# Optimization experiments

Hardware: AMD Instinct MI355X
Metric: run time of the kernel (lower is better)

The kernel has to match this reference:

```python
import jax, jax.numpy as jnp
import numpy as np

H = 8          # head_count
C = 512        # emb_dim
DH = C // H    # head_emb_size = 64
FF = 4 * C     # feed_forward hidden = 2048
EPS = 1e-5     # nn.LayerNorm default eps


def setup_inputs() -> dict:
    key = jax.random.key(0)
    ks = jax.random.split(key, 16)
    s = lambda fan_in: 1.0 / np.sqrt(fan_in)
    inp = {
        "x": jax.random.normal(ks[0], (4, 2048, C), dtype=jnp.float32),
        "ln1_g": jnp.ones((C,), jnp.float32),
        "ln1_b": jnp.zeros((C,), jnp.float32),
        # per-head QKV projections, stacked over heads: [H, C, DH]
        "Wq": jax.random.uniform(ks[1], (H, C, DH), jnp.float32, -s(C), s(C)),
        "bq": jax.random.uniform(ks[2], (H, DH), jnp.float32, -s(C), s(C)),
        "Wk": jax.random.uniform(ks[3], (H, C, DH), jnp.float32, -s(C), s(C)),
        "bk": jax.random.uniform(ks[4], (H, DH), jnp.float32, -s(C), s(C)),
        "Wv": jax.random.uniform(ks[5], (H, C, DH), jnp.float32, -s(C), s(C)),
        "bv": jax.random.uniform(ks[6], (H, DH), jnp.float32, -s(C), s(C)),
        "Wp": jax.random.uniform(ks[7], (C, C), jnp.float32, -s(C), s(C)),
        "bp": jax.random.uniform(ks[8], (C,), jnp.float32, -s(C), s(C)),
        "ln2_g": jnp.ones((C,), jnp.float32),
        "ln2_b": jnp.zeros((C,), jnp.float32),
        "W1": jax.random.uniform(ks[9], (C, FF), jnp.float32, -s(C), s(C)),
        "b1": jax.random.uniform(ks[10], (FF,), jnp.float32, -s(C), s(C)),
        "W2": jax.random.uniform(ks[11], (FF, C), jnp.float32, -s(FF), s(FF)),
        "b2": jax.random.uniform(ks[12], (C,), jnp.float32, -s(FF), s(FF)),
    }
    return inp


def _layernorm(x, g, b):
    mu = jnp.mean(x, axis=-1, keepdims=True)
    var = jnp.mean((x - mu) ** 2, axis=-1, keepdims=True)
    return (x - mu) * jax.lax.rsqrt(var + EPS) * g + b


def _block(x, ln1_g, ln1_b, Wq, bq, Wk, bk, Wv, bv, Wp, bp, ln2_g, ln2_b, W1, b1, W2, b2):
    B, T, _ = x.shape
    h = _layernorm(x, ln1_g, ln1_b)
    # per-head projections, vectorized over heads: [B,H,T,DH]
    Q = jnp.einsum("btc,hcd->bhtd", h, Wq) + bq[None, :, None, :]
    K = jnp.einsum("btc,hcd->bhtd", h, Wk) + bk[None, :, None, :]
    V = jnp.einsum("btc,hcd->bhtd", h, Wv) + bv[None, :, None, :]
    wei = jnp.einsum("bhtd,bhsd->bhts", Q, K) / jnp.sqrt(jnp.float32(DH))
    causal = jnp.tril(jnp.ones((T, T), dtype=bool))
    wei = jnp.where(causal, wei, jnp.float32(-1e9))  # masked_fill(-1e9)
    wei = jax.nn.softmax(wei, axis=-1)
    out = jnp.einsum("bhts,bhsd->bhtd", wei, V)      # [B,H,T,DH]
    # concat heads (head order = ModuleList order) -> [B,T,C]
    out = out.transpose(0, 2, 1, 3).reshape(B, T, H * DH)
    attn = out @ Wp + bp
    x = x + attn
    h2 = _layernorm(x, ln2_g, ln2_b)
    ff = jax.nn.relu(h2 @ W1 + b1) @ W2 + b2
    return x + ff


def reference(x, ln1_g, ln1_b, Wq, bq, Wk, bk, Wv, bv, Wp, bp, ln2_g, ln2_b, W1, b1, W2, b2):
    return _block(x, ln1_g, ln1_b, Wq, bq, Wk, bk, Wv, bv, Wp, bp, ln2_g, ln2_b, W1, b1, W2, b2)
```

## Files before the change

### kernel.cpp

```cpp
#include <hip/hip_runtime.h>

typedef unsigned short u16;
typedef unsigned int   u32;
typedef __attribute__((ext_vector_type(4))) int   i32x4;
typedef __attribute__((ext_vector_type(4))) float f32x4;
typedef __attribute__((ext_vector_type(4))) unsigned short u16x4;
typedef __attribute__((ext_vector_type(8))) unsigned short u16x8;

#define DEVI static __device__ __forceinline__

DEVI u16 f2b(float f) {
  u32 u = __builtin_bit_cast(u32, f);
  return (u16)((u + 0x7FFFu + ((u >> 16) & 1u)) >> 16);
}

DEVI void mfma16(f32x4& d, i32x4 a, i32x4 b) {
  asm("v_mfma_f32_16x16x32_bf16 %0, %1, %2, %0" : "+v"(d) : "v"(a), "v"(b));
}

DEVI void gload16(const void* g, void* l) {
  __builtin_amdgcn_global_load_lds(
      (const __attribute__((address_space(1))) void*)g,
      (__attribute__((address_space(3))) void*)l, 16, 0, 0);
}

DEVI int swz(int row, int b) {
  return (row << 7) + (((b >> 4) ^ (row & 7)) << 4) + (b & 15);
}

__global__ __launch_bounds__(256) void trans_tile(
    const float* __restrict__ src, u16* __restrict__ dst, int R, int C)
{
  __shared__ u16 tile[64][72];
  const int rb = blockIdx.x * 64, cb = blockIdx.y * 64;
  const int t = threadIdx.x;
  const int tr = t >> 2, tc = (t & 3) * 16;
  const float* sp = src + (size_t)(rb + tr) * C + cb + tc;
  #pragma unroll
  for (int q = 0; q < 4; q++) {
    float4 v = *(const float4*)(sp + q * 4);
    tile[tr][tc + q*4 + 0] = f2b(v.x);
    tile[tr][tc + q*4 + 1] = f2b(v.y);
    tile[tr][tc + q*4 + 2] = f2b(v.z);
    tile[tr][tc + q*4 + 3] = f2b(v.w);
  }
  __syncthreads();
  const int dc = t >> 2, dr = (t & 3) * 16;
  u16x8 o0, o1;
  #pragma unroll
  for (int j = 0; j < 8; j++) { o0[j] = tile[dr + j][dc]; o1[j] = tile[dr + 8 + j][dc]; }
  u16* dp = dst + (size_t)(cb + dc) * R + rb + dr;
  *(u16x8*)(dp) = o0;
  *(u16x8*)(dp + 8) = o1;
}

__global__ __launch_bounds__(256) void pack_qkv_tile(
    const float* __restrict__ Wq, const float* __restrict__ Wk,
    const float* __restrict__ Wv, u16* __restrict__ dst)
{
  __shared__ u16 tile[64][72];
  const int bid = blockIdx.x;
  const int cb = (bid & 7) * 64, h = (bid >> 3) & 7, widx = bid >> 6;
  const float* W = (widx == 0) ? Wq : (widx == 1) ? Wk : Wv;
  const float* src = W + (size_t)h * 512 * 64;
  const int t = threadIdx.x;
  const int tr = t >> 2, tc = (t & 3) * 16;
  const float* sp = src + (size_t)(cb + tr) * 64 + tc;
  #pragma unroll
  for (int q = 0; q < 4; q++) {
    float4 v = *(const float4*)(sp + q * 4);
    tile[tr][tc + q*4 + 0] = f2b(v.x);
    tile[tr][tc + q*4 + 1] = f2b(v.y);
    tile[tr][tc + q*4 + 2] = f2b(v.z);
    tile[tr][tc + q*4 + 3] = f2b(v.w);
  }
  __syncthreads();
  const int dc = t >> 2, dr = (t & 3) * 16;
  u16x8 o0, o1;
  #pragma unroll
  for (int j = 0; j < 8; j++) { o0[j] = tile[dr + j][dc]; o1[j] = tile[dr + 8 + j][dc]; }
  u16* dp = dst + (size_t)(widx * 512 + h * 64 + dc) * 512 + cb + dr;
  *(u16x8*)(dp) = o0;
  *(u16x8*)(dp + 8) = o1;
}

__global__ __launch_bounds__(256) void ln_kernel(
    const float* __restrict__ x, const float* __restrict__ gamma,
    const float* __restrict__ beta, u16* __restrict__ out)
{
  const int lane = threadIdx.x & 63;
  const int row = blockIdx.x * 4 + (threadIdx.x >> 6);
  const float4* xr = (const float4*)(x + (size_t)row * 512) + lane * 2;
  float4 a0 = xr[0], a1 = xr[1];
  float s  = a0.x + a0.y + a0.z + a0.w + a1.x + a1.y + a1.z + a1.w;
  float sq = a0.x*a0.x + a0.y*a0.y + a0.z*a0.z + a0.w*a0.w
           + a1.x*a1.x + a1.y*a1.y + a1.z*a1.z + a1.w*a1.w;
  #pragma unroll
  for (int o = 32; o > 0; o >>= 1) { s += __shfl_xor(s, o); sq += __shfl_xor(sq, o); }
  const float mu = s * (1.0f / 512.0f);
  const float rstd = rsqrtf(sq * (1.0f / 512.0f) - mu * mu + 1e-5f);
  const float4* g4 = (const float4*)gamma + lane * 2;
  const float4* b4 = (const float4*)beta  + lane * 2;
  float4 g0 = g4[0], g1 = g4[1], b0 = b4[0], b1 = b4[1];
  float xv[8] = {a0.x,a0.y,a0.z,a0.w,a1.x,a1.y,a1.z,a1.w};
  float gv[8] = {g0.x,g0.y,g0.z,g0.w,g1.x,g1.y,g1.z,g1.w};
  float bv[8] = {b0.x,b0.y,b0.z,b0.w,b1.x,b1.y,b1.z,b1.w};
  u16x8 ov;
  #pragma unroll
  for (int j = 0; j < 8; j++) ov[j] = f2b((xv[j] - mu) * rstd * gv[j] + bv[j]);
  *(u16x8*)(out + (size_t)row * 512 + lane * 8) = ov;
}

template<int KD, int EPI>
__global__ __launch_bounds__(256) void gemm_bt(
    const u16* __restrict__ A, const u16* __restrict__ Bt,
    const float* __restrict__ bias0, const float* __restrict__ bias1,
    const float* __restrict__ bias2, const float* __restrict__ resid,
    void* __restrict__ out0, void* __restrict__ out1, void* __restrict__ out2)
{
  __shared__ __align__(16) u16 sA[3][128 * 32];
  __shared__ __align__(16) u16 sB[3][128 * 32];
  constexpr int NSTEP = KD / 32;
  const int tid = threadIdx.x, lane = tid & 63, w = tid >> 6;
  const int m0 = blockIdx.x * 128, n0 = blockIdx.y * 128;
  const int wr = w >> 1, wc = w & 1, r = lane & 15, gq = lane >> 4;

  f32x4 acc[4][4] = {};

  const int o0 = w * 2048 + lane * 16;
  const int row0 = o0 >> 6, kb0 = o0 & 63;
  const int o1 = o0 + 1024;
  const int row1 = o1 >> 6, kb1 = o1 & 63;
  const char* Ab = (const char*)A;
  const char* Bb = (const char*)Bt;

#define STAGE(step, buf) do {                                                \
    const int kbyte_ = (step) * 64;                                          \
    char* sAd_ = (char*)sA + (buf) * 8192 + w * 2048;                        \
    char* sBd_ = (char*)sB + (buf) * 8192 + w * 2048;                        \
    gload16(Ab + (size_t)(m0 + row0) * (KD * 2) + kbyte_ + kb0, sAd_);       \
    gload16(Ab + (size_t)(m0 + row1) * (KD * 2) + kbyte_ + kb1, sAd_ + 1024);\
    gload16(Bb + (size_t)(n0 + row0) * (KD * 2) + kbyte_ + kb0, sBd_);       \
    gload16(Bb + (size_t)(n0 + row1) * (KD * 2) + kbyte_ + kb1, sBd_ + 1024);\
  } while (0)

  STAGE(0, 0);
  STAGE(1, 1);

  for (int t = 0; t < NSTEP; t++) {
    __builtin_amdgcn_sched_barrier(0);
    __builtin_amdgcn_s_barrier();
    if (t + 2 < NSTEP) {
      STAGE(t + 2, (t + 2) % 3);
      asm volatile("s_waitcnt vmcnt(8)" ::: "memory");
    } else if (t + 1 < NSTEP) {
      asm volatile("s_waitcnt vmcnt(4)" ::: "memory");
    } else {
      asm volatile("s_waitcnt vmcnt(0)" ::: "memory");
    }
    __builtin_amdgcn_sched_barrier(0);
    __builtin_amdgcn_s_barrier();
    const u16* sAc = sA[t % 3];
    const u16* sBc = sB[t % 3];
    i32x4 af[4], bfr[4];
    #pragma unroll
    for (int i = 0; i < 4; i++)
      af[i] = *(const i32x4*)(sAc + (wr * 64 + i * 16 + r) * 32 + gq * 8);
    #pragma unroll
    for (int j = 0; j < 4; j++)
      bfr[j] = *(const i32x4*)(sBc + (wc * 64 + j * 16 + r) * 32 + gq * 8);
    #pragma unroll
    for (int i = 0; i < 4; i++)
      #pragma unroll
      for (int j = 0; j < 4; j++)
        mfma16(acc[i][j], af[i], bfr[j]);
  }
#undef STAGE

  #pragma unroll
  for (int i = 0; i < 4; i++) {
    #pragma unroll
    for (int j = 0; j < 4; j++) {
      const int mb = m0 + wr * 64 + i * 16 + gq * 4;
      const int nc = n0 + wc * 64 + j * 16 + r;
      #pragma unroll
      for (int e = 0; e < 4; e++) {
        const int m = mb + e;
        float v = acc[i][j][e];
        if (EPI == 0) {
          float bias; u16* dst;
          if (nc < 512)       { bias = bias0[nc];        dst = (u16*)out0; }
          else if (nc < 1024) { bias = bias1[nc - 512];  dst = (u16*)out1; }
          else                { bias = bias2[nc - 1024]; dst = (u16*)out2; }
          v += bias;
          const int nn = nc & 511, h = nn >> 6, d = nn & 63;
          const int bb = m >> 11, tt = m & 2047;
          dst[(size_t)((bb * 8 + h) * 2048 + tt) * 64 + d] = f2b(v);
        } else if (EPI == 1) {
          v += bias0[nc] + resid[(size_t)m * 512 + nc];
          ((float*)out0)[(size_t)m * 512 + nc] = v;
        } else {
          v += bias0[nc];
          v = fmaxf(v, 0.0f);
          ((u16*)out0)[(size_t)m * 2048 + nc] = f2b(v);
        }
      }
    }
  }
}

__global__ __launch_bounds__(256) void attn_kernel(
    const u16* __restrict__ Q, const u16* __restrict__ K,
    const u16* __restrict__ V, u16* __restrict__ O)
{
  __shared__ __align__(16) char lds[40960];
  const int tid = threadIdx.x, lane = tid & 63, w = tid >> 6;
  const int p = blockIdx.x & 15, bh = blockIdx.x >> 4;
  const int r = lane & 15, gq = lane >> 4;
  const u16* Qb = Q + (size_t)bh * (2048 * 64);
  const u16* Kb = K + (size_t)bh * (2048 * 64);
  const u16* Vb = V + (size_t)bh * (2048 * 64);
  const int bb = bh >> 3, hh = bh & 7;
  char* Pb = lds + 32768 + w * 2048;

  const int sv = (tid & 15) * 4;
  const int dv = (tid >> 4) * 4;
  u16x4 vr[4];

#define STAGEK(s0g, buf) do {                                              \
    _Pragma("unroll")                                                      \
    for (int i_ = 0; i_ < 2; i_++) {                                       \
      int o_ = w * 2048 + i_ * 1024 + lane * 16;                           \
      int so_ = o_ ^ (((o_ >> 7) & 7) << 4);                               \
      gload16((const char*)(Kb + (size_t)(s0g) * 64) + so_,                \
              lds + (buf) * 8192 + w * 2048 + i_ * 1024);                  \
    } } while (0)

#define LOADV(s0g) do {                                                    \
    _Pragma("unroll")                                                      \
    for (int j_ = 0; j_ < 4; j_++)                                         \
      vr[j_] = *(const u16x4*)(Vb + (size_t)((s0g) + sv + j_) * 64 + dv);  \
    } while (0)

#define WRITEV(buf) do {                                                   \
    _Pragma("unroll")                                                      \
    for (int dd_ = 0; dd_ < 4; dd_++) {                                    \
      u16x4 val_ = {vr[0][dd_], vr[1][dd_], vr[2][dd_], vr[3][dd_]};       \
      *(u16x4*)(lds + 16384 + (buf) * 8192 + swz(dv + dd_, sv * 2)) = val_;\
    } } while (0)

  #pragma unroll 1
  for (int half = 0; half < 2; half++) {
    const int qt = half ? p : (31 - p);
    const int q0 = qt << 6;
    const int qg = q0 + w * 16 + r;

    i32x4 qf[2];
    qf[0] = *(const i32x4*)(Qb + (size_t)(q0 + w * 16 + r) * 64 + gq * 8);
    qf[1] = *(const i32x4*)(Qb + (size_t)(q0 + w * 16 + r) * 64 + 32 + gq * 8);

    STAGEK(0, 0);
    LOADV(0);
    WRITEV(0);
    __syncthreads();

    f32x4 accO[4] = {};
    float m_run = -1e30f, l_run = 0.0f;

    for (int t = 0; t <= qt; t++) {
      const int cb = t & 1, nb = cb ^ 1;
      const bool diag = (t == qt);
      const int s0 = t << 6;
      if (!diag) {
        STAGEK(s0 + 64, nb);
        LOADV(s0 + 64);
      }

      f32x4 st[4] = {};
      const int sbmax = diag ? (w + 1) : 4;
      #pragma unroll
      for (int kd = 0; kd < 2; kd++)
        #pragma unroll
        for (int sb = 0; sb < 4; sb++)
          if (sb < sbmax) {
            i32x4 kf = *(const i32x4*)(lds + cb * 8192 + swz(sb * 16 + r, kd * 64 + gq * 16));
            mfma16(st[sb], kf, qf[kd]);
          }

      float tmax = -1e30f;
      if (diag) {
        #pragma unroll
        for (int sb = 0; sb < 4; sb++)
          #pragma unroll
          for (int e = 0; e < 4; e++) {
            int sg = s0 + sb * 16 + gq * 4 + e;
            float v = st[sb][e] * 0.125f;
            v = (sg <= qg) ? v : -1e30f;
            st[sb][e] = v;
            tmax = fmaxf(tmax, v);
          }
      } else {
        #pragma unroll
        for (int sb = 0; sb < 4; sb++)
          #pragma unroll
          for (int e = 0; e < 4; e++) {
            float v = st[sb][e] * 0.125f;
            st[sb][e] = v;
            tmax = fmaxf(tmax, v);
          }
      }
      tmax = fmaxf(tmax, __shfl_xor(tmax, 16));
      tmax = fmaxf(tmax, __shfl_xor(tmax, 32));

      if (!__all(tmax <= m_run)) {
        const float mnew = fmaxf(m_run, tmax);
        const float alpha = __expf(m_run - mnew);
        l_run *= alpha;
        float ae[4];
        #pragma unroll
        for (int e = 0; e < 4; e++) ae[e] = __shfl(alpha, gq * 4 + e);
        #pragma unroll
        for (int db = 0; db < 4; db++)
          #pragma unroll
          for (int e = 0; e < 4; e++) accO[db][e] *= ae[e];
        m_run = mnew;
      }
      float rsum = 0.0f;
      #pragma unroll
      for (int sb = 0; sb < 4; sb++)
        #pragma unroll
        for (int e = 0; e < 4; e++) {
          float pv = __expf(st[sb][e] - m_run);
          st[sb][e] = pv;
          rsum += pv;
        }
      rsum += __shfl_xor(rsum, 16);
      rsum += __shfl_xor(rsum, 32);
      l_run += rsum;

      #pragma unroll
      for (int sb = 0; sb < 4; sb++) {
        u32 lo, hi;
        asm("v_cvt_pk_bf16_f32 %0, %1, %2" : "=v"(lo) : "v"(st[sb][0]), "v"(st[sb][1]));
        asm("v_cvt_pk_bf16_f32 %0, %1, %2" : "=v"(hi) : "v"(st[sb][2]), "v"(st[sb][3]));
        uint2 pk; pk.x = lo; pk.y = hi;
        *(uint2*)(Pb + swz(r, sb * 32 + gq * 8)) = pk;
      }

      const int kmax = diag ? ((w >> 1) + 1) : 2;
      #pragma unroll
      for (int ks = 0; ks < 2; ks++)
        if (ks < kmax) {
          i32x4 pf = *(const i32x4*)(Pb + swz(r, ks * 64 + gq * 16));
          #pragma unroll
          for (int db = 0; db < 4; db++) {
            i32x4 vf = *(const i32x4*)(lds + 16384 + cb * 8192 + swz(db * 16 + r, ks * 64 + gq * 16));
            mfma16(accO[db], pf, vf);
          }
        }

      if (!diag) WRITEV(nb);
      __syncthreads();
    }

    float le[4];
    #pragma unroll
    for (int e = 0; e < 4; e++) le[e] = 1.0f / __shfl(l_run, gq * 4 + e);
    #pragma unroll
    for (int db = 0; db < 4; db++)
      #pragma unroll
      for (int e = 0; e < 4; e++) {
        int qrow = q0 + w * 16 + gq * 4 + e;
        int d = db * 16 + r;
        O[(size_t)(bb * 2048 + qrow) * 512 + hh * 64 + d] = f2b(accO[db][e] * le[e]);
      }
  }
#undef STAGEK
#undef LOADV
#undef WRITEV
}

extern "C" void kernel_launch(void* const* d_in, const int* in_sizes, int n_in,
                              void* d_out, int out_size, void* d_ws, size_t ws_size,
                              hipStream_t stream)
{
  const float* x    = (const float*)d_in[0];
  const float* ln1g = (const float*)d_in[1];
  const float* ln1b = (const float*)d_in[2];
  const float* Wq   = (const float*)d_in[3];
  const float* bq   = (const float*)d_in[4];
  const float* Wk   = (const float*)d_in[5];
  const float* bk   = (const float*)d_in[6];
  const float* Wv   = (const float*)d_in[7];
  const float* bv   = (const float*)d_in[8];
  const float* Wp   = (const float*)d_in[9];
  const float* bp   = (const float*)d_in[10];
  const float* ln2g = (const float*)d_in[11];
  const float* ln2b = (const float*)d_in[12];
  const float* W1   = (const float*)d_in[13];
  const float* b1   = (const float*)d_in[14];
  const float* W2   = (const float*)d_in[15];
  const float* b2   = (const float*)d_in[16];

  char* ws = (char*)d_ws;
  const size_t MB = 1ull << 20;
  float* x1  = (float*)(ws);
  u16* hbuf  = (u16*)(ws + 16 * MB);
  u16* Qb    = (u16*)(ws + 24 * MB);
  u16* Kb    = (u16*)(ws + 32 * MB);
  u16* Vb    = (u16*)(ws + 40 * MB);
  u16* attn  = (u16*)(ws + 48 * MB);
  u16* fbuf  = (u16*)(ws + 24 * MB);
  u16* Wqkv  = (u16*)(ws + 56 * MB);
  u16* Wpt   = (u16*)(ws + 58 * MB);
  u16* W1t   = (u16*)(ws + 59 * MB);
  u16* W2t   = (u16*)(ws + 61 * MB);
  float* outf = (float*)d_out;

  pack_qkv_tile<<<192, 256, 0, stream>>>(Wq, Wk, Wv, Wqkv);
  trans_tile<<<dim3(8, 8),  256, 0, stream>>>(Wp, Wpt, 512, 512);
  trans_tile<<<dim3(8, 32), 256, 0, stream>>>(W1, W1t, 512, 2048);
  trans_tile<<<dim3(32, 8), 256, 0, stream>>>(W2, W2t, 2048, 512);
  ln_kernel<<<2048, 256, 0, stream>>>(x, ln1g, ln1b, hbuf);
  gemm_bt<512, 0><<<dim3(64, 12), 256, 0, stream>>>(hbuf, Wqkv, bq, bk, bv,
                                                    nullptr, Qb, Kb, Vb);
  attn_kernel<<<512, 256, 0, stream>>>(Qb, Kb, Vb, attn);
  gemm_bt<512, 1><<<dim3(64, 4), 256, 0, stream>>>(attn, Wpt, bp, nullptr, nullptr,
                                                   x, x1, nullptr, nullptr);
  ln_kernel<<<2048, 256, 0, stream>>>(x1, ln2g, ln2b, hbuf);
  gemm_bt<512, 2><<<dim3(64, 16), 256, 0, stream>>>(hbuf, W1t, b1, nullptr, nullptr,
                                                    nullptr, fbuf, nullptr, nullptr);
  gemm_bt<2048, 1><<<dim3(64, 4), 256, 0, stream>>>(fbuf, W2t, b2, nullptr, nullptr,
                                                    x1, outf, nullptr, nullptr);
}
```

Measured before the change: 177.6 us.

## Remap GEMM blocks across XCDs, raise MFMA priority, use exp2 in softmax

GEMM launches move to a 1D grid with a block-index remap, so consecutive tiles that share A rows land on the same XCD chiplet and hit its L2. The MFMA loop is wrapped in s_setprio to favour matrix issue over other waves. In attention, the softmax scale folds in log2(e) and exp is computed with the hardware v_exp_f32 (exp2) instead of __expf, saving a multiply per element. The remap assumes the grid size is a multiple of 8. The raw v_exp_f32 may handle denormals or extreme inputs slightly differently.

```diff
diff --git a/kernel.cpp b/kernel.cpp
--- a/kernel.cpp
+++ b/kernel.cpp
@@ -12,6 +12,12 @@
 DEVI u16 f2b(float f) {
   u32 u = __builtin_bit_cast(u32, f);
   return (u16)((u + 0x7FFFu + ((u >> 16) & 1u)) >> 16);
+}
+
+DEVI float exp2_hw(float x) {
+  float r;
+  asm("v_exp_f32 %0, %1" : "=v"(r) : "v"(x));
+  return r;
 }
 
 DEVI void mfma16(f32x4& d, i32x4 a, i32x4 b) {
@@ -111,7 +117,7 @@
   *(u16x8*)(out + (size_t)row * 512 + lane * 8) = ov;
 }
 
-template<int KD, int EPI>
+template<int KD, int NT, int EPI>
 __global__ __launch_bounds__(256) void gemm_bt(
     const u16* __restrict__ A, const u16* __restrict__ Bt,
     const float* __restrict__ bias0, const float* __restrict__ bias1,
@@ -121,8 +127,10 @@
   __shared__ __align__(16) u16 sA[3][128 * 32];
   __shared__ __align__(16) u16 sB[3][128 * 32];
   constexpr int NSTEP = KD / 32;
+  constexpr int CPX = (64 * NT) / 8;
   const int tid = threadIdx.x, lane = tid & 63, w = tid >> 6;
-  const int m0 = blockIdx.x * 128, n0 = blockIdx.y * 128;
+  const int wg = (blockIdx.x & 7) * CPX + (blockIdx.x >> 3);
+  const int m0 = (wg / NT) * 128, n0 = (wg % NT) * 128;
   const int wr = w >> 1, wc = w & 1, r = lane & 15, gq = lane >> 4;
 
   f32x4 acc[4][4] = {};
@@ -169,11 +177,13 @@
     #pragma unroll
     for (int j = 0; j < 4; j++)
       bfr[j] = *(const i32x4*)(sBc + (wc * 64 + j * 16 + r) * 32 + gq * 8);
+    __builtin_amdgcn_s_setprio(1);
     #pragma unroll
     for (int i = 0; i < 4; i++)
       #pragma unroll
       for (int j = 0; j < 4; j++)
         mfma16(acc[i][j], af[i], bfr[j]);
+    __builtin_amdgcn_s_setprio(0);
   }
 #undef STAGE
 
@@ -226,6 +236,7 @@
   const int sv = (tid & 15) * 4;
   const int dv = (tid >> 4) * 4;
   u16x4 vr[4];
+  const float SC2 = 0.125f * 1.44269504f;
 
 #define STAGEK(s0g, buf) do {                                              \
     _Pragma("unroll")                                                      \
@@ -294,7 +305,7 @@
           #pragma unroll
           for (int e = 0; e < 4; e++) {
             int sg = s0 + sb * 16 + gq * 4 + e;
-            float v = st[sb][e] * 0.125f;
+            float v = st[sb][e] * SC2;
             v = (sg <= qg) ? v : -1e30f;
             st[sb][e] = v;
             tmax = fmaxf(tmax, v);
@@ -304,7 +315,7 @@
         for (int sb = 0; sb < 4; sb++)
           #pragma unroll
           for (int e = 0; e < 4; e++) {
-            float v = st[sb][e] * 0.125f;
+            float v = st[sb][e] * SC2;
             st[sb][e] = v;
             tmax = fmaxf(tmax, v);
           }
@@ -314,7 +325,7 @@
 
       if (!__all(tmax <= m_run)) {
         const float mnew = fmaxf(m_run, tmax);
-        const float alpha = __expf(m_run - mnew);
+        const float alpha = exp2_hw(m_run - mnew);
         l_run *= alpha;
         float ae[4];
         #pragma unroll
@@ -330,7 +341,7 @@
       for (int sb = 0; sb < 4; sb++)
         #pragma unroll
         for (int e = 0; e < 4; e++) {
-          float pv = __expf(st[sb][e] - m_run);
+          float pv = exp2_hw(st[sb][e] - m_run);
           st[sb][e] = pv;
           rsum += pv;
         }
@@ -422,14 +433,14 @@
   trans_tile<<<dim3(8, 32), 256, 0, stream>>>(W1, W1t, 512, 2048);
   trans_tile<<<dim3(32, 8), 256, 0, stream>>>(W2, W2t, 2048, 512);
   ln_kernel<<<2048, 256, 0, stream>>>(x, ln1g, ln1b, hbuf);
-  gemm_bt<512, 0><<<dim3(64, 12), 256, 0, stream>>>(hbuf, Wqkv, bq, bk, bv,
-                                                    nullptr, Qb, Kb, Vb);
+  gemm_bt<512, 12, 0><<<768, 256, 0, stream>>>(hbuf, Wqkv, bq, bk, bv,
+                                               nullptr, Qb, Kb, Vb);
   attn_kernel<<<512, 256, 0, stream>>>(Qb, Kb, Vb, attn);
-  gemm_bt<512, 1><<<dim3(64, 4), 256, 0, stream>>>(attn, Wpt, bp, nullptr, nullptr,
-                                                   x, x1, nullptr, nullptr);
+  gemm_bt<512, 4, 1><<<256, 256, 0, stream>>>(attn, Wpt, bp, nullptr, nullptr,
+                                              x, x1, nullptr, nullptr);
   ln_kernel<<<2048, 256, 0, stream>>>(x1, ln2g, ln2b, hbuf);
-  gemm_bt<512, 2><<<dim3(64, 16), 256, 0, stream>>>(hbuf, W1t, b1, nullptr, nullptr,
-                                                    nullptr, fbuf, nullptr, nullptr);
-  gemm_bt<2048, 1><<<dim3(64, 4), 256, 0, stream>>>(fbuf, W2t, b2, nullptr, nullptr,
-                                                    x1, outf, nullptr, nullptr);
-}
+  gemm_bt<512, 16, 2><<<1024, 256, 0, stream>>>(hbuf, W1t, b1, nullptr, nullptr,
+                                                nullptr, fbuf, nullptr, nullptr);
+  gemm_bt<2048, 4, 1><<<256, 256, 0, stream>>>(fbuf, W2t, b2, nullptr, nullptr,
+                                               x1, outf, nullptr, nullptr);
+}
```

Result: no change. 178.9 us (+0.7%).
